# Kernel optimization log

Hardware: AMD Instinct MI355X
Metric: run time of the kernel (lower is better)

Reference implementation:

```python
import jax, jax.numpy as jnp
import numpy as np

# ---- static module configuration ----
N_POU = 16
N_BC = 3
P = N_POU + N_BC          # full_n_pou = 19
F = 3                      # n_fields
B, N, D_IN, D_Z, D_H = 16, 1024, 32, 64, 64
N_DIR = 64
MAX_ITERS = 50
ALPHA = 0.1                # damped fixed-point step of the nonlinear solver

# edge_pairs / delta_0 for the complete graph on P POU nodes (construct_delta0)
_ei, _ej = np.triu_indices(P, 1)
E = _ei.shape[0]           # n_one_forms = P*(P-1)/2 = 171
_d0 = np.zeros((E, P), np.float32)
_d0[np.arange(E), _ei] = -1.0
_d0[np.arange(E), _ej] = 1.0
DELTA0 = jnp.asarray(_d0)  # [E, P]
EI = jnp.asarray(_ei)
EJ = jnp.asarray(_ej)


def setup_inputs() -> dict:
    key = jax.random.key(0)
    ks = jax.random.split(key, 16)
    f32 = jnp.float32
    inp = {
        'in_tokens': jax.random.normal(ks[0], (B, N, D_IN), f32),
        'K_list': 0.02 * jax.random.normal(ks[1], (B, F, N, N), f32),
        'M_list': 0.02 * jax.random.normal(ks[2], (B, F, N, N), f32),
        'dirichlet_nodes': jax.random.randint(ks[3], (B, N_DIR), 0, N),
        'boundary_vals': jax.random.normal(ks[4], (B, N_DIR, F), f32),
        'u_init': jax.random.normal(ks[5], (B, P * F), f32),
        # learned parameters (encoder / source_model / boundary_w / flux_model)
        'W_enc': jax.random.normal(ks[6], (D_IN, D_Z), f32) / np.sqrt(D_IN),
        'b_enc': jnp.zeros((D_Z,), f32),
        'W_src': jax.random.normal(ks[7], (D_Z, F), f32) / np.sqrt(D_Z),
        'b_src': jnp.zeros((F,), f32),
        'W_pou': jax.random.normal(ks[8], (D_Z, P * F), f32) / np.sqrt(D_Z),
        'Wf1': jax.random.normal(ks[9], (2 * F, D_H), f32) / np.sqrt(2 * F),
        'Wz': jax.random.normal(ks[10], (D_Z, D_H), f32) / np.sqrt(D_Z),
        'bf': jnp.zeros((D_H,), f32),
        'Wf2': 0.1 * jax.random.normal(ks[11], (D_H, F), f32) / np.sqrt(D_H),
    }
    return inp


def reference(in_tokens, K_list, M_list, dirichlet_nodes, boundary_vals, u_init,
              W_enc, b_enc, W_src, b_src, W_pou, Wf1, Wz, bf, Wf2):
    Bc, Nn = in_tokens.shape[0], in_tokens.shape[1]
    latent_scaling = Nn / P

    # encoder: in_tokens -> per-node latents z [B,N,Dz]
    z = jnp.tanh(in_tokens @ W_enc + b_enc)

    # boundary_w: partition-of-unity weights W [B,P,N,F], boundary POUs biased
    # toward Dirichlet nodes via boundary_vals
    logits = (z @ W_pou).reshape(Bc, Nn, P, F)
    bidx = jnp.arange(Bc)[:, None]
    bvals_full = jnp.zeros((Bc, Nn, F), in_tokens.dtype).at[bidx, dirichlet_nodes].set(boundary_vals)
    logits = logits.at[:, :, P - N_BC:, :].add(bvals_full[:, :, None, :])
    Wmat = jax.nn.softmax(logits, axis=2).transpose(0, 2, 1, 3)  # [B,P,N,F]

    # source_model + latent projection (source_mode='identity' -> pass-through)
    f_full = z @ W_src + b_src                                    # [B,N,F]
    f_latent = jnp.einsum('bpif,bif->bpf', Wmat, f_full) / latent_scaling

    # project_bilinear_per_field: K_hat[b,p,q,f] = W K W^T / scaling
    def project(Kl):
        t = jnp.einsum('bpif,bfij->bpjf', Wmat, Kl)               # [B,P,N,F]
        return jnp.einsum('bpjf,bqjf->bpqf', t, Wmat) / latent_scaling

    # apply_dirichlet_per_field: boundary rows -> identity
    eyeP = jnp.eye(P, dtype=in_tokens.dtype)
    row_mask = jnp.zeros((P,), bool).at[P - N_BC:].set(True)
    def dirichlet_bilinear(Kh):
        return jnp.where(row_mask[None, :, None, None], eyeP[None, :, :, None], Kh)

    K_hat = dirichlet_bilinear(project(K_list))                   # [B,P,P,F]
    M_hat = dirichlet_bilinear(project(M_list))

    bc_mask = jnp.zeros((P, F), bool).at[P - N_BC:, :].set(True)
    bc_vals = jnp.zeros((P, F), in_tokens.dtype).at[P - N_BC, :].set(1.0)

    # flux_model conditioning: pooled latent, precomputed once
    zp = jnp.mean(z, axis=1) @ Wz                                 # [B,Dh]
    src_term = jnp.einsum('bpqf,bqf->bpf', M_hat, f_latent)       # constant in u

    def G(u_flat):  # G_residual
        u = u_flat.reshape(Bc, P, F)
        diff_term = jnp.einsum('bpqf,bqf->bpf', K_hat, u)
        ue = jnp.concatenate([u[:, EI], u[:, EJ]], axis=-1)       # [B,E,2F]
        flux = jnp.tanh(ue @ Wf1 + zp[:, None, :] + bf) @ Wf2     # [B,E,F]
        flux_term = jnp.einsum('ep,bef->bpf', DELTA0, flux)
        r = diff_term - src_term - flux_term
        r = jnp.where(bc_mask[None], u - bc_vals[None], r)        # Dirichlet residual
        return r.reshape(Bc, -1)

    # NonlinearSolver: damped fixed-point iteration, fixed MAX_ITERS under jit
    def step(u, _):
        return u - ALPHA * G(u), None
    u_hat, _ = jax.lax.scan(step, u_init, None, length=MAX_ITERS)

    u_coarse = u_hat.reshape(Bc, P, F)
    u_fine = jnp.einsum('bpif,bpf->bif', Wmat, u_coarse)          # [B,N,F]
    return u_fine
```

## Files before the change

kernel.cpp:

```cpp
#include <hip/hip_runtime.h>

#define Bn 16
#define Nn 1024
#define DIN 32
#define DZ 64
#define Fc 3
#define Pp 19
#define PPAD 20
#define Ee 171
#define ITERS 50
#define INV_SCALE (19.0f/1024.0f)
#define CHUNK 64
#define PF 4
#define PFK 8

#define OFF_WPROJ 0
#define OFF_FFULL 983040
#define OFF_FLAT  1033216
#define OFF_UBUF  1034128
#define OFF_BVALS 1035040
#define OFF_ZACC  1084192
#define OFF_KHAT  1085216
#define OFF_SRC   1099808
#define ZERO_FLOATS 65536
#define OFF_TPART 1100576
#define NEED_FLOATS (OFF_TPART + 48*16*16*1024)

__global__ __launch_bounds__(1024) void k_scatter(const int* __restrict__ nodes,
                                                  const float* __restrict__ bvals,
                                                  float* __restrict__ bfull) {
  __shared__ int sn[1024];
  int tid = threadIdx.x;
  sn[tid] = nodes[tid];
  __syncthreads();
  int b = tid >> 6, j = tid & 63;
  int node = sn[tid];
  bool win = true;
  for (int j2 = j + 1; j2 < 64; j2++)
    if (sn[(b << 6) | j2] == node) { win = false; break; }
  if (win) {
    #pragma unroll
    for (int f = 0; f < Fc; f++)
      bfull[((size_t)b*Nn + node)*Fc + f] = bvals[(size_t)tid*Fc + f];
  }
}

__global__ __launch_bounds__(128) void k_encode(
    const float* __restrict__ x, const float* __restrict__ Wenc, const float* __restrict__ benc,
    const float* __restrict__ Wsrc, const float* __restrict__ bsrc, const float* __restrict__ Wpou,
    const float* __restrict__ bfull, float* __restrict__ wproj, float* __restrict__ ffull,
    float* __restrict__ zacc) {
  __shared__ float sWenc[DIN*DZ];
  __shared__ float sWpou[DZ*57];
  __shared__ float sWsrc[DZ*Fc];
  int tid = threadIdx.x;
  for (int t = tid; t < DIN*DZ; t += 128) sWenc[t] = Wenc[t];
  for (int t = tid; t < DZ*57; t += 128) sWpou[t] = Wpou[t];
  for (int t = tid; t < DZ*Fc; t += 128) sWsrc[t] = Wsrc[t];
  __syncthreads();
  int g = blockIdx.x*128 + tid;
  int b = g >> 10, i = g & 1023;
  float xr[DIN];
  const float* xp = x + (size_t)g*DIN;
  #pragma unroll
  for (int k = 0; k < DIN; k += 4) {
    float4 t4 = *(const float4*)(xp + k);
    xr[k] = t4.x; xr[k+1] = t4.y; xr[k+2] = t4.z; xr[k+3] = t4.w;
  }
  float l[57];
  #pragma unroll
  for (int o = 0; o < 57; o++) l[o] = 0.f;
  float ff[3] = {bsrc[0], bsrc[1], bsrc[2]};
  int lane = tid & 63;
  for (int d = 0; d < DZ; d++) {
    float zd = benc[d];
    #pragma unroll
    for (int k = 0; k < DIN; k++) zd = fmaf(xr[k], sWenc[k*DZ + d], zd);
    zd = tanhf(zd);
    #pragma unroll
    for (int o = 0; o < 57; o++) l[o] = fmaf(zd, sWpou[d*57 + o], l[o]);
    #pragma unroll
    for (int f = 0; f < Fc; f++) ff[f] = fmaf(zd, sWsrc[d*Fc + f], ff[f]);
    float zs = zd;
    #pragma unroll
    for (int off = 32; off > 0; off >>= 1) zs += __shfl_xor(zs, off, 64);
    if (lane == 0) atomicAdd(&zacc[b*DZ + d], zs);
  }
  #pragma unroll
  for (int f = 0; f < Fc; f++) ffull[(size_t)g*Fc + f] = ff[f];
  #pragma unroll
  for (int f = 0; f < Fc; f++) {
    float bv = bfull[(size_t)g*Fc + f];
    l[16*3+f] += bv; l[17*3+f] += bv; l[18*3+f] += bv;
  }
  #pragma unroll
  for (int f = 0; f < Fc; f++) {
    float m = l[f];
    #pragma unroll
    for (int p = 1; p < Pp; p++) m = fmaxf(m, l[p*3+f]);
    float ex[Pp]; float s = 0.f;
    #pragma unroll
    for (int p = 0; p < Pp; p++) { ex[p] = __expf(l[p*3+f] - m); s += ex[p]; }
    float inv = 1.f / s;
    float* wp = wproj + ((size_t)(b*Fc + f)*Nn + i)*PPAD;
    #pragma unroll
    for (int p = 0; p < Pp; p++) wp[p] = ex[p]*inv;
  }
}

__global__ __launch_bounds__(256) void k_flat(const float* __restrict__ wproj,
                                              const float* __restrict__ ffull,
                                              float* __restrict__ flat) {
  int bf = blockIdx.x;
  int b = bf / 3, f = bf % 3;
  float acc[Pp];
  #pragma unroll
  for (int q = 0; q < Pp; q++) acc[q] = 0.f;
  for (int i = threadIdx.x; i < Nn; i += 256) {
    float fv = ffull[((size_t)b*Nn + i)*Fc + f];
    const float* row = wproj + ((size_t)bf*Nn + i)*PPAD;
    #pragma unroll
    for (int q = 0; q < Pp; q++) acc[q] = fmaf(row[q], fv, acc[q]);
  }
  #pragma unroll
  for (int q = 0; q < Pp; q++) {
    float v = acc[q];
    #pragma unroll
    for (int off = 32; off > 0; off >>= 1) v += __shfl_xor(v, off, 64);
    acc[q] = v;
  }
  __shared__ float red[4][Pp];
  int wave = threadIdx.x >> 6, lane = threadIdx.x & 63;
  if (lane == 0) {
    #pragma unroll
    for (int q = 0; q < Pp; q++) red[wave][q] = acc[q];
  }
  __syncthreads();
  if (threadIdx.x < Pp) {
    float s = red[0][threadIdx.x] + red[1][threadIdx.x] + red[2][threadIdx.x] + red[3][threadIdx.x];
    flat[bf*Pp + threadIdx.x] = s * INV_SCALE;
  }
}

__global__ __launch_bounds__(256, 3) void k_projT(
    const float* __restrict__ Kl, const float* __restrict__ wproj,
    float* __restrict__ tpart) {
  __shared__ float sW[16*CHUNK];
  int chunk = blockIdx.x;
  int bf = blockIdx.y;
  int i0 = chunk * CHUNK;
  const float* Kb = Kl + (size_t)bf*Nn*Nn + (size_t)i0*Nn;
  const float* Wrow0 = wproj + ((size_t)bf*Nn + i0)*PPAD;
  int tid = threadIdx.x;
  for (int t = tid; t < 16*CHUNK; t += 256) {
    int r = t & (CHUNK-1), p = t >> 6;
    sW[p*CHUNK + r] = Wrow0[r*PPAD + p];
  }
  __syncthreads();
  int j0 = tid * 4;
  float4 acc[16];
  #pragma unroll
  for (int p = 0; p < 16; p++) { acc[p].x = 0.f; acc[p].y = 0.f; acc[p].z = 0.f; acc[p].w = 0.f; }
  const float* kp = Kb + j0;
  float4 kbuf[PFK];
  #pragma unroll
  for (int s = 0; s < PFK; s++) kbuf[s] = *(const float4*)(kp + (size_t)s*Nn);
  for (int ii = 0; ii < CHUNK; ii += PFK) {
    #pragma unroll
    for (int s = 0; s < PFK; s++) {
      float4 k4 = kbuf[s];
      int nxt = (ii + PFK + s) & (CHUNK - 1);
      kbuf[s] = *(const float4*)(kp + (size_t)nxt*Nn);
      const float* wrow = &sW[ii + s];
      #pragma unroll
      for (int p = 0; p < 16; p++) {
        float wv = wrow[p*CHUNK];
        acc[p].x = fmaf(wv, k4.x, acc[p].x);
        acc[p].y = fmaf(wv, k4.y, acc[p].y);
        acc[p].z = fmaf(wv, k4.z, acc[p].z);
        acc[p].w = fmaf(wv, k4.w, acc[p].w);
      }
    }
  }
  float* tp = tpart + ((size_t)(bf*16 + chunk)*16)*Nn + j0;
  #pragma unroll
  for (int p = 0; p < 16; p++) *(float4*)(tp + (size_t)p*Nn) = acc[p];
}

__global__ __launch_bounds__(256, 3) void k_projM(
    const float* __restrict__ Ml, const float* __restrict__ wproj,
    const float* __restrict__ flat, float* __restrict__ srca) {
  __shared__ float sW[16*CHUNK];
  int chunk = blockIdx.x;
  int bf = blockIdx.y;
  int i0 = chunk * CHUNK;
  const float* Mb = Ml + (size_t)bf*Nn*Nn + (size_t)i0*Nn;
  const float* Wp = wproj + (size_t)bf*Nn*PPAD;
  const float* Wrow0 = Wp + (size_t)i0*PPAD;
  int tid = threadIdx.x;
  for (int t = tid; t < 16*CHUNK; t += 256) {
    int r = t & (CHUNK-1), p = t >> 6;
    sW[p*CHUNK + r] = Wrow0[r*PPAD + p];
  }
  float fl[Pp];
  #pragma unroll
  for (int q = 0; q < Pp; q++) fl[q] = flat[bf*Pp + q];
  int j0 = tid * 4;
  float v0, v1, v2, v3;
  {
    float vv[4];
    #pragma unroll
    for (int r = 0; r < 4; r++) {
      const float* row = Wp + (size_t)(j0 + r)*PPAD;
      float s = 0.f;
      #pragma unroll
      for (int q = 0; q < Pp; q++) s = fmaf(row[q], fl[q], s);
      vv[r] = s;
    }
    v0 = vv[0]; v1 = vv[1]; v2 = vv[2]; v3 = vv[3];
  }
  __syncthreads();
  float sa[16];
  #pragma unroll
  for (int p = 0; p < 16; p++) sa[p] = 0.f;
  const float* mp = Mb + j0;
  float4 mbuf[PFK];
  #pragma unroll
  for (int s = 0; s < PFK; s++) mbuf[s] = *(const float4*)(mp + (size_t)s*Nn);
  for (int ii = 0; ii < CHUNK; ii += PFK) {
    #pragma unroll
    for (int s = 0; s < PFK; s++) {
      float4 m4 = mbuf[s];
      int nxt = (ii + PFK + s) & (CHUNK - 1);
      mbuf[s] = *(const float4*)(mp + (size_t)nxt*Nn);
      float tm = m4.x*v0 + m4.y*v1 + m4.z*v2 + m4.w*v3;
      const float* wrow = &sW[ii + s];
      #pragma unroll
      for (int p = 0; p < 16; p++) sa[p] = fmaf(wrow[p*CHUNK], tm, sa[p]);
    }
  }
  int lane = tid & 63;
  #pragma unroll
  for (int p = 0; p < 16; p++) {
    float vq = sa[p];
    #pragma unroll
    for (int off = 32; off > 0; off >>= 1) vq += __shfl_xor(vq, off, 64);
    sa[p] = vq;
  }
  if (lane == 0) {
    #pragma unroll
    for (int p = 0; p < 16; p++) atomicAdd(&srca[bf*16 + p], sa[p] * INV_SCALE);
  }
}

__global__ __launch_bounds__(256) void k_khat(const float* __restrict__ tpart,
                                              const float* __restrict__ wproj,
                                              float* __restrict__ khat) {
  __shared__ float sT[16*64];
  __shared__ float sWq[64*PPAD];
  int jb = blockIdx.x, bf = blockIdx.y;
  int tid = threadIdx.x;
  {
    int id = tid * 4;
    int p = id >> 6;
    int r = id & 63;
    const float* base = tpart + ((size_t)(bf*16)*16 + p)*Nn + jb*64 + r;
    float4 s4 = make_float4(0.f, 0.f, 0.f, 0.f);
    #pragma unroll 4
    for (int c = 0; c < 16; c++) {
      float4 t4 = *(const float4*)(base + (size_t)c*16*Nn);
      s4.x += t4.x; s4.y += t4.y; s4.z += t4.z; s4.w += t4.w;
    }
    *(float4*)&sT[p*64 + r] = s4;
  }
  const float* wsrc = wproj + ((size_t)bf*Nn + jb*64)*PPAD;
  for (int t = tid; t < 64*PPAD; t += 256) sWq[t] = wsrc[t];
  __syncthreads();
  for (int o = tid; o < 16*Pp; o += 256) {
    int p = o / Pp, q = o - p*Pp;
    float s = 0.f;
    #pragma unroll
    for (int r = 0; r < 64; r++) s = fmaf(sT[p*64 + r], sWq[r*PPAD + q], s);
    atomicAdd(&khat[(bf*16 + p)*Pp + q], s * INV_SCALE);
  }
}

__global__ __launch_bounds__(256, 1) void k_project_fb(
    const float* __restrict__ Kl, const float* __restrict__ Ml,
    const float* __restrict__ wproj, const float* __restrict__ flat,
    float* __restrict__ khat, float* __restrict__ srca) {
  __shared__ float sW[16*CHUNK];
  int chunk = blockIdx.x;
  int bf = blockIdx.y;
  int i0 = chunk * CHUNK;
  const float* Kb = Kl + (size_t)bf*Nn*Nn + (size_t)i0*Nn;
  const float* Mb = Ml + (size_t)bf*Nn*Nn + (size_t)i0*Nn;
  const float* Wp = wproj + (size_t)bf*Nn*PPAD;
  const float* Wrow0 = Wp + (size_t)i0*PPAD;
  int tid = threadIdx.x;
  for (int t = tid; t < 16*CHUNK; t += 256) {
    int r = t & (CHUNK-1), p = t >> 6;
    sW[p*CHUNK + r] = Wrow0[r*PPAD + p];
  }
  float fl[Pp];
  #pragma unroll
  for (int q = 0; q < Pp; q++) fl[q] = flat[bf*Pp + q];
  int j0 = tid * 4;
  float v[4];
  #pragma unroll
  for (int r = 0; r < 4; r++) {
    const float* row = Wp + (size_t)(j0 + r)*PPAD;
    float s = 0.f;
    #pragma unroll
    for (int q = 0; q < Pp; q++) s = fmaf(row[q], fl[q], s);
    v[r] = s;
  }
  __syncthreads();
  float4 acc[16];
  float sa[16];
  #pragma unroll
  for (int p = 0; p < 16; p++) {
    acc[p].x = 0.f; acc[p].y = 0.f; acc[p].z = 0.f; acc[p].w = 0.f;
    sa[p] = 0.f;
  }
  const float* kp = Kb + j0;
  const float* mp = Mb + j0;
  float4 kbuf[PF], mbuf[PF];
  #pragma unroll
  for (int s = 0; s < PF; s++) {
    kbuf[s] = *(const float4*)(kp + (size_t)s*Nn);
    mbuf[s] = *(const float4*)(mp + (size_t)s*Nn);
  }
  for (int ii = 0; ii < CHUNK; ii += PF) {
    #pragma unroll
    for (int s = 0; s < PF; s++) {
      float4 k4 = kbuf[s], m4 = mbuf[s];
      int nxt = (ii + PF + s) & (CHUNK - 1);
      kbuf[s] = *(const float4*)(kp + (size_t)nxt*Nn);
      mbuf[s] = *(const float4*)(mp + (size_t)nxt*Nn);
      float tm = m4.x*v[0] + m4.y*v[1] + m4.z*v[2] + m4.w*v[3];
      const float* wrow = &sW[ii + s];
      #pragma unroll
      for (int p = 0; p < 16; p++) {
        float wv = wrow[p*CHUNK];
        acc[p].x = fmaf(wv, k4.x, acc[p].x);
        acc[p].y = fmaf(wv, k4.y, acc[p].y);
        acc[p].z = fmaf(wv, k4.z, acc[p].z);
        acc[p].w = fmaf(wv, k4.w, acc[p].w);
        sa[p] = fmaf(wv, tm, sa[p]);
      }
    }
  }
  int lane = tid & 63;
  #pragma unroll
  for (int q = 0; q < Pp; q++) {
    float w0 = Wp[(size_t)(j0 + 0)*PPAD + q];
    float w1 = Wp[(size_t)(j0 + 1)*PPAD + q];
    float w2 = Wp[(size_t)(j0 + 2)*PPAD + q];
    float w3 = Wp[(size_t)(j0 + 3)*PPAD + q];
    float pr[16];
    #pragma unroll
    for (int p = 0; p < 16; p++)
      pr[p] = acc[p].x*w0 + acc[p].y*w1 + acc[p].z*w2 + acc[p].w*w3;
    #pragma unroll
    for (int p = 0; p < 16; p++) {
      float vq = pr[p];
      #pragma unroll
      for (int off = 32; off > 0; off >>= 1) vq += __shfl_xor(vq, off, 64);
      pr[p] = vq;
    }
    if (lane == 0) {
      #pragma unroll
      for (int p = 0; p < 16; p++)
        atomicAdd(&khat[(bf*16 + p)*Pp + q], pr[p] * INV_SCALE);
    }
  }
  #pragma unroll
  for (int p = 0; p < 16; p++) {
    float vq = sa[p];
    #pragma unroll
    for (int off = 32; off > 0; off >>= 1) vq += __shfl_xor(vq, off, 64);
    sa[p] = vq;
  }
  if (lane == 0) {
    #pragma unroll
    for (int p = 0; p < 16; p++) atomicAdd(&srca[bf*16 + p], sa[p] * INV_SCALE);
  }
}

__global__ __launch_bounds__(384, 1) void k_solve(
    const float* __restrict__ khat, const float* __restrict__ srca,
    const float* __restrict__ zacc, const float* __restrict__ Wz,
    const float* __restrict__ u_init, const float* __restrict__ Wf1,
    const float* __restrict__ bfv, const float* __restrict__ Wf2,
    float* __restrict__ ubuf) {
  int b = blockIdx.x;
  __shared__ float u4[Pp*4];
  __shared__ float flux_s[Ee*Fc];
  __shared__ float sW1p[DZ*8];
  __shared__ float sW2p[DZ*4];
  __shared__ float sK[Fc*16*Pp];
  __shared__ float ssrc[Fc*16];
  int tid = threadIdx.x;
  for (int t = tid; t < 6*DZ; t += 384) {
    int k = t >> 6, d = t & 63;
    sW1p[d*8 + k] = 2.f * Wf1[t];
  }
  for (int t = tid; t < DZ*Fc; t += 384) {
    int d = t / 3, c = t - d*3;
    sW2p[d*4 + c] = Wf2[t];
  }
  if (tid < DZ) {
    float s = 0.f;
    for (int k = 0; k < DZ; k++) s = fmaf(zacc[b*DZ + k], Wz[k*DZ + tid], s);
    sW1p[tid*8 + 6] = 2.f * (bfv[tid] + s * (1.f/1024.f));
    sW1p[tid*8 + 7] = 0.f;
    sW2p[tid*4 + 3] = 0.f;
  }
  for (int t = tid; t < Fc*16*Pp; t += 384) sK[t] = khat[b*Fc*16*Pp + t];
  if (tid < 48) ssrc[tid] = srca[b*48 + tid];
  if (tid < 57) u4[(tid/3)*4 + (tid%3)] = u_init[b*57 + tid];
  if (tid < Pp) u4[tid*4 + 3] = 0.f;
  __syncthreads();
  int e = tid >> 1, h = tid & 1;
  bool active = (e < Ee);
  int ei = 0, ej = 0;
  if (active) {
    int r = e, i = 0;
    while (r >= 18 - i) { r -= 18 - i; i++; }
    ei = i; ej = i + 1 + r;
  }
  int d0 = h * 32;
  bool upd = (tid < 57);
  int up = tid / 3, uf = tid - (tid/3)*3;
  for (int it = 0; it < ITERS; it++) {
    if (active) {
      float4 ua = *(const float4*)&u4[ei*4];
      float4 ub = *(const float4*)&u4[ej*4];
      float fl0 = 0.f, fl1 = 0.f, fl2 = 0.f;
      #pragma unroll 16
      for (int dd = 0; dd < 32; dd++) {
        int d = d0 + dd;
        float4 wA = *(const float4*)&sW1p[d*8];
        float4 wB = *(const float4*)&sW1p[d*8 + 4];
        float pre = wB.z;
        pre = fmaf(ua.x, wA.x, pre);
        pre = fmaf(ua.y, wA.y, pre);
        pre = fmaf(ua.z, wA.z, pre);
        pre = fmaf(ub.x, wA.w, pre);
        pre = fmaf(ub.y, wB.x, pre);
        pre = fmaf(ub.z, wB.y, pre);
        float t = __expf(pre);
        float r = __builtin_amdgcn_rcpf(t + 1.f);
        float th = fmaf(-2.f, r, 1.f);
        float4 w2 = *(const float4*)&sW2p[d*4];
        fl0 = fmaf(th, w2.x, fl0);
        fl1 = fmaf(th, w2.y, fl1);
        fl2 = fmaf(th, w2.z, fl2);
      }
      fl0 += __shfl_xor(fl0, 1, 64);
      fl1 += __shfl_xor(fl1, 1, 64);
      fl2 += __shfl_xor(fl2, 1, 64);
      if (h == 0) { flux_s[e*3+0] = fl0; flux_s[e*3+1] = fl1; flux_s[e*3+2] = fl2; }
    }
    __syncthreads();
    if (upd) {
      float u_old = u4[up*4 + uf];
      float r_;
      if (up < 16) {
        float diff = 0.f;
        const float* kr = &sK[(uf*16 + up)*Pp];
        for (int q = 0; q < Pp; q++) diff = fmaf(kr[q], u4[q*4 + uf], diff);
        float ft = 0.f;
        for (int o = 0; o < Pp; o++) {
          if (o == up) continue;
          int i_ = (o < up) ? o : up;
          int j_ = (o < up) ? up : o;
          int eidx = i_*Pp - (i_*(i_+1))/2 + (j_ - i_ - 1);
          float sgn = (o < up) ? 1.f : -1.f;
          ft += sgn * flux_s[eidx*3 + uf];
        }
        r_ = diff - ssrc[uf*16 + up] - ft;
      } else {
        r_ = u_old - ((up == 16) ? 1.f : 0.f);
      }
      u4[up*4 + uf] = u_old - 0.1f * r_;
    }
    __syncthreads();
  }
  if (tid < 57) ubuf[b*57 + tid] = u4[(tid/3)*4 + (tid%3)];
}

__global__ __launch_bounds__(256) void k_out(const float* __restrict__ wproj,
                                             const float* __restrict__ ubuf,
                                             float* __restrict__ out) {
  __shared__ float u_s[57];
  int b = blockIdx.y;
  int i = blockIdx.x*256 + threadIdx.x;
  if (threadIdx.x < 57) u_s[threadIdx.x] = ubuf[b*57 + threadIdx.x];
  __syncthreads();
  #pragma unroll
  for (int f = 0; f < Fc; f++) {
    const float* row = wproj + ((size_t)(b*Fc + f)*Nn + i)*PPAD;
    float s = 0.f;
    #pragma unroll
    for (int p = 0; p < Pp; p++) s = fmaf(row[p], u_s[p*3 + f], s);
    out[((size_t)b*Nn + i)*Fc + f] = s;
  }
}

extern "C" void kernel_launch(void* const* d_in, const int* in_sizes, int n_in,
                              void* d_out, int out_size, void* d_ws, size_t ws_size,
                              hipStream_t stream) {
  const float* in_tokens = (const float*)d_in[0];
  const float* K_list    = (const float*)d_in[1];
  const float* M_list    = (const float*)d_in[2];
  const int*   dnodes    = (const int*)d_in[3];
  const float* bvals     = (const float*)d_in[4];
  const float* u_init    = (const float*)d_in[5];
  const float* W_enc     = (const float*)d_in[6];
  const float* b_enc     = (const float*)d_in[7];
  const float* W_src     = (const float*)d_in[8];
  const float* b_src     = (const float*)d_in[9];
  const float* W_pou     = (const float*)d_in[10];
  const float* Wf1       = (const float*)d_in[11];
  const float* Wz        = (const float*)d_in[12];
  const float* bfv       = (const float*)d_in[13];
  const float* Wf2       = (const float*)d_in[14];
  float* ws  = (float*)d_ws;
  float* out = (float*)d_out;

  float* WPROJ = ws + OFF_WPROJ;
  float* FFULL = ws + OFF_FFULL;
  float* FLAT  = ws + OFF_FLAT;
  float* UBUF  = ws + OFF_UBUF;
  float* BVALS = ws + OFF_BVALS;
  float* ZACC  = ws + OFF_ZACC;
  float* KHAT  = ws + OFF_KHAT;
  float* SRC   = ws + OFF_SRC;
  float* TPART = ws + OFF_TPART;

  hipMemsetAsync(ws + OFF_BVALS, 0, (size_t)ZERO_FLOATS * sizeof(float), stream);
  k_scatter<<<1, 1024, 0, stream>>>(dnodes, bvals, BVALS);
  k_encode<<<128, 128, 0, stream>>>(in_tokens, W_enc, b_enc, W_src, b_src, W_pou,
                                    BVALS, WPROJ, FFULL, ZACC);
  k_flat<<<Bn*Fc, 256, 0, stream>>>(WPROJ, FFULL, FLAT);
  if (ws_size >= (size_t)NEED_FLOATS * sizeof(float)) {
    k_projT<<<dim3(Nn/CHUNK, Bn*Fc), 256, 0, stream>>>(K_list, WPROJ, TPART);
    k_projM<<<dim3(Nn/CHUNK, Bn*Fc), 256, 0, stream>>>(M_list, WPROJ, FLAT, SRC);
    k_khat<<<dim3(16, Bn*Fc), 256, 0, stream>>>(TPART, WPROJ, KHAT);
  } else {
    k_project_fb<<<dim3(Nn/CHUNK, Bn*Fc), 256, 0, stream>>>(K_list, M_list, WPROJ, FLAT, KHAT, SRC);
  }
  k_solve<<<Bn, 384, 0, stream>>>(KHAT, SRC, ZACC, Wz, u_init, Wf1, bfv, Wf2, UBUF);
  k_out<<<dim3(Nn/256, Bn), 256, 0, stream>>>(WPROJ, UBUF, out);
}
```

Before: 787.7 us.

## Keep flux MLP weights in registers and split edges across 8-lane groups

The solve kernel now gives each lane a fixed 8-wide slice of the hidden dimension and keeps the Wf1, bias and Wf2 weights for that slice in registers. Each group of 8 lanes processes one edge per round, over 6 rounds, with a 3-step shuffle reduction. This removes the per-iteration LDS weight loads and shrinks the block from 384 to 256 threads. The residual loops are also unrolled. In exchange the kernel uses more registers and does more shuffles per edge, and some lanes sit idle in the last round.

```diff
diff --git a/kernel.cpp b/kernel.cpp
--- a/kernel.cpp
+++ b/kernel.cpp
@@ -388,7 +388,7 @@
   }
 }
 
-__global__ __launch_bounds__(384, 1) void k_solve(
+__global__ __launch_bounds__(256, 1) void k_solve(
     const float* __restrict__ khat, const float* __restrict__ srca,
     const float* __restrict__ zacc, const float* __restrict__ Wz,
     const float* __restrict__ u_init, const float* __restrict__ Wf1,
@@ -397,71 +397,84 @@
   int b = blockIdx.x;
   __shared__ float u4[Pp*4];
   __shared__ float flux_s[Ee*Fc];
-  __shared__ float sW1p[DZ*8];
-  __shared__ float sW2p[DZ*4];
+  __shared__ float sbz[DZ];
   __shared__ float sK[Fc*16*Pp];
   __shared__ float ssrc[Fc*16];
   int tid = threadIdx.x;
-  for (int t = tid; t < 6*DZ; t += 384) {
-    int k = t >> 6, d = t & 63;
-    sW1p[d*8 + k] = 2.f * Wf1[t];
-  }
-  for (int t = tid; t < DZ*Fc; t += 384) {
-    int d = t / 3, c = t - d*3;
-    sW2p[d*4 + c] = Wf2[t];
-  }
   if (tid < DZ) {
     float s = 0.f;
     for (int k = 0; k < DZ; k++) s = fmaf(zacc[b*DZ + k], Wz[k*DZ + tid], s);
-    sW1p[tid*8 + 6] = 2.f * (bfv[tid] + s * (1.f/1024.f));
-    sW1p[tid*8 + 7] = 0.f;
-    sW2p[tid*4 + 3] = 0.f;
-  }
-  for (int t = tid; t < Fc*16*Pp; t += 384) sK[t] = khat[b*Fc*16*Pp + t];
+    sbz[tid] = bfv[tid] + s * (1.f/1024.f);
+  }
+  for (int t = tid; t < Fc*16*Pp; t += 256) sK[t] = khat[b*Fc*16*Pp + t];
   if (tid < 48) ssrc[tid] = srca[b*48 + tid];
   if (tid < 57) u4[(tid/3)*4 + (tid%3)] = u_init[b*57 + tid];
   if (tid < Pp) u4[tid*4 + 3] = 0.f;
   __syncthreads();
-  int e = tid >> 1, h = tid & 1;
-  bool active = (e < Ee);
-  int ei = 0, ej = 0;
-  if (active) {
-    int r = e, i = 0;
+
+  int wave = tid >> 6, lane = tid & 63;
+  int g = lane >> 3, sub = lane & 7;
+  int dbase = sub * 8;
+  float w1r[6][8];
+  #pragma unroll
+  for (int k = 0; k < 6; k++)
+    #pragma unroll
+    for (int j = 0; j < 8; j++) w1r[k][j] = 2.f * Wf1[k*DZ + dbase + j];
+  float bzr[8];
+  #pragma unroll
+  for (int j = 0; j < 8; j++) bzr[j] = 2.f * sbz[dbase + j];
+  float w2r[3][8];
+  #pragma unroll
+  for (int j = 0; j < 8; j++) {
+    w2r[0][j] = Wf2[(dbase + j)*3 + 0];
+    w2r[1][j] = Wf2[(dbase + j)*3 + 1];
+    w2r[2][j] = Wf2[(dbase + j)*3 + 2];
+  }
+  int e_[6], ei_[6], ej_[6];
+  bool act_[6];
+  #pragma unroll
+  for (int rd = 0; rd < 6; rd++) {
+    int e = rd*32 + wave*8 + g;
+    act_[rd] = (e < Ee);
+    int r = act_[rd] ? e : 0, i = 0;
     while (r >= 18 - i) { r -= 18 - i; i++; }
-    ei = i; ej = i + 1 + r;
-  }
-  int d0 = h * 32;
+    e_[rd] = e; ei_[rd] = i; ej_[rd] = i + 1 + r;
+  }
   bool upd = (tid < 57);
   int up = tid / 3, uf = tid - (tid/3)*3;
+
   for (int it = 0; it < ITERS; it++) {
-    if (active) {
-      float4 ua = *(const float4*)&u4[ei*4];
-      float4 ub = *(const float4*)&u4[ej*4];
-      float fl0 = 0.f, fl1 = 0.f, fl2 = 0.f;
-      #pragma unroll 16
-      for (int dd = 0; dd < 32; dd++) {
-        int d = d0 + dd;
-        float4 wA = *(const float4*)&sW1p[d*8];
-        float4 wB = *(const float4*)&sW1p[d*8 + 4];
-        float pre = wB.z;
-        pre = fmaf(ua.x, wA.x, pre);
-        pre = fmaf(ua.y, wA.y, pre);
-        pre = fmaf(ua.z, wA.z, pre);
-        pre = fmaf(ub.x, wA.w, pre);
-        pre = fmaf(ub.y, wB.x, pre);
-        pre = fmaf(ub.z, wB.y, pre);
-        float t = __expf(pre);
-        float r = __builtin_amdgcn_rcpf(t + 1.f);
-        float th = fmaf(-2.f, r, 1.f);
-        float4 w2 = *(const float4*)&sW2p[d*4];
-        fl0 = fmaf(th, w2.x, fl0);
-        fl1 = fmaf(th, w2.y, fl1);
-        fl2 = fmaf(th, w2.z, fl2);
+    #pragma unroll
+    for (int rd = 0; rd < 6; rd++) {
+      if (act_[rd]) {
+        float4 ua = *(const float4*)&u4[ei_[rd]*4];
+        float4 ub = *(const float4*)&u4[ej_[rd]*4];
+        float fl0 = 0.f, fl1 = 0.f, fl2 = 0.f;
+        #pragma unroll
+        for (int j = 0; j < 8; j++) {
+          float pre = bzr[j];
+          pre = fmaf(ua.x, w1r[0][j], pre);
+          pre = fmaf(ua.y, w1r[1][j], pre);
+          pre = fmaf(ua.z, w1r[2][j], pre);
+          pre = fmaf(ub.x, w1r[3][j], pre);
+          pre = fmaf(ub.y, w1r[4][j], pre);
+          pre = fmaf(ub.z, w1r[5][j], pre);
+          float t = __expf(pre);
+          float rr = __builtin_amdgcn_rcpf(t + 1.f);
+          float th = fmaf(-2.f, rr, 1.f);
+          fl0 = fmaf(th, w2r[0][j], fl0);
+          fl1 = fmaf(th, w2r[1][j], fl1);
+          fl2 = fmaf(th, w2r[2][j], fl2);
+        }
+        fl0 += __shfl_xor(fl0, 1, 64); fl0 += __shfl_xor(fl0, 2, 64); fl0 += __shfl_xor(fl0, 4, 64);
+        fl1 += __shfl_xor(fl1, 1, 64); fl1 += __shfl_xor(fl1, 2, 64); fl1 += __shfl_xor(fl1, 4, 64);
+        fl2 += __shfl_xor(fl2, 1, 64); fl2 += __shfl_xor(fl2, 2, 64); fl2 += __shfl_xor(fl2, 4, 64);
+        if (sub == 0) {
+          flux_s[e_[rd]*3 + 0] = fl0;
+          flux_s[e_[rd]*3 + 1] = fl1;
+          flux_s[e_[rd]*3 + 2] = fl2;
+        }
       }
-      fl0 += __shfl_xor(fl0, 1, 64);
-      fl1 += __shfl_xor(fl1, 1, 64);
-      fl2 += __shfl_xor(fl2, 1, 64);
-      if (h == 0) { flux_s[e*3+0] = fl0; flux_s[e*3+1] = fl1; flux_s[e*3+2] = fl2; }
     }
     __syncthreads();
     if (upd) {
@@ -470,8 +483,10 @@
       if (up < 16) {
         float diff = 0.f;
         const float* kr = &sK[(uf*16 + up)*Pp];
+        #pragma unroll
         for (int q = 0; q < Pp; q++) diff = fmaf(kr[q], u4[q*4 + uf], diff);
         float ft = 0.f;
+        #pragma unroll
         for (int o = 0; o < Pp; o++) {
           if (o == up) continue;
           int i_ = (o < up) ? o : up;
@@ -552,6 +567,6 @@
   } else {
     k_project_fb<<<dim3(Nn/CHUNK, Bn*Fc), 256, 0, stream>>>(K_list, M_list, WPROJ, FLAT, KHAT, SRC);
   }
-  k_solve<<<Bn, 384, 0, stream>>>(KHAT, SRC, ZACC, Wz, u_init, Wf1, bfv, Wf2, UBUF);
+  k_solve<<<Bn, 256, 0, stream>>>(KHAT, SRC, ZACC, Wz, u_init, Wf1, bfv, Wf2, UBUF);
   k_out<<<dim3(Nn/256, Bn), 256, 0, stream>>>(WPROJ, UBUF, out);
 }
```

Measured after the change: 733.9 us. -6.8%, faster.

## Pack flux MLP weights per batch and read them as wave-uniform scalar loads

Applied to the files above, without the earlier changes.

A new small kernel precomputes the per-batch flux weights (Wf1, the conditioned bias and Wf2) into a packed 16-float-per-hidden-unit layout in global memory. The solver remaps threads so that each wave handles 64 edges over one half of the hidden dimension, making the weight address wave-uniform so it can be served by scalar loads instead of LDS reads. It also drops the cross-lane shuffle reduction, writing two partial flux buffers that the update step sums. The update loops are unrolled. This adds one kernel launch and depends on the compiler actually emitting scalar loads for the weights.

```diff
diff --git a/kernel.cpp b/kernel.cpp
--- a/kernel.cpp
+++ b/kernel.cpp
@@ -13,6 +13,7 @@
 #define CHUNK 64
 #define PF 4
 #define PFK 8
+#define WPACK_B 1024
 
 #define OFF_WPROJ 0
 #define OFF_FFULL 983040
@@ -23,7 +24,8 @@
 #define OFF_KHAT  1085216
 #define OFF_SRC   1099808
 #define ZERO_FLOATS 65536
-#define OFF_TPART 1100576
+#define OFF_WPACK 1100576
+#define OFF_TPART 1116960
 #define NEED_FLOATS (OFF_TPART + 48*16*16*1024)
 
 __global__ __launch_bounds__(1024) void k_scatter(const int* __restrict__ nodes,
@@ -140,6 +142,25 @@
     float s = red[0][threadIdx.x] + red[1][threadIdx.x] + red[2][threadIdx.x] + red[3][threadIdx.x];
     flat[bf*Pp + threadIdx.x] = s * INV_SCALE;
   }
+}
+
+__global__ __launch_bounds__(64) void k_wpack(
+    const float* __restrict__ zacc, const float* __restrict__ Wz,
+    const float* __restrict__ bfv, const float* __restrict__ Wf1,
+    const float* __restrict__ Wf2, float* __restrict__ wpack) {
+  int b = blockIdx.x, d = threadIdx.x;
+  float s = 0.f;
+  for (int k = 0; k < DZ; k++) s = fmaf(zacc[b*DZ + k], Wz[k*DZ + d], s);
+  float bz = bfv[d] + s * (1.f/1024.f);
+  float* w = wpack + (size_t)b*WPACK_B + d*16;
+  #pragma unroll
+  for (int k = 0; k < 6; k++) w[k] = 2.f * Wf1[k*DZ + d];
+  w[6] = 2.f * bz;
+  w[7] = 0.f;
+  w[8]  = Wf2[d*3 + 0];
+  w[9]  = Wf2[d*3 + 1];
+  w[10] = Wf2[d*3 + 2];
+  w[11] = 0.f; w[12] = 0.f; w[13] = 0.f; w[14] = 0.f; w[15] = 0.f;
 }
 
 __global__ __launch_bounds__(256, 3) void k_projT(
@@ -390,78 +411,63 @@
 
 __global__ __launch_bounds__(384, 1) void k_solve(
     const float* __restrict__ khat, const float* __restrict__ srca,
-    const float* __restrict__ zacc, const float* __restrict__ Wz,
-    const float* __restrict__ u_init, const float* __restrict__ Wf1,
-    const float* __restrict__ bfv, const float* __restrict__ Wf2,
+    const float* __restrict__ wpack, const float* __restrict__ u_init,
     float* __restrict__ ubuf) {
   int b = blockIdx.x;
   __shared__ float u4[Pp*4];
-  __shared__ float flux_s[Ee*Fc];
-  __shared__ float sW1p[DZ*8];
-  __shared__ float sW2p[DZ*4];
+  __shared__ float fluxp[2][Ee*3];
   __shared__ float sK[Fc*16*Pp];
   __shared__ float ssrc[Fc*16];
   int tid = threadIdx.x;
-  for (int t = tid; t < 6*DZ; t += 384) {
-    int k = t >> 6, d = t & 63;
-    sW1p[d*8 + k] = 2.f * Wf1[t];
-  }
-  for (int t = tid; t < DZ*Fc; t += 384) {
-    int d = t / 3, c = t - d*3;
-    sW2p[d*4 + c] = Wf2[t];
-  }
-  if (tid < DZ) {
-    float s = 0.f;
-    for (int k = 0; k < DZ; k++) s = fmaf(zacc[b*DZ + k], Wz[k*DZ + tid], s);
-    sW1p[tid*8 + 6] = 2.f * (bfv[tid] + s * (1.f/1024.f));
-    sW1p[tid*8 + 7] = 0.f;
-    sW2p[tid*4 + 3] = 0.f;
-  }
   for (int t = tid; t < Fc*16*Pp; t += 384) sK[t] = khat[b*Fc*16*Pp + t];
   if (tid < 48) ssrc[tid] = srca[b*48 + tid];
   if (tid < 57) u4[(tid/3)*4 + (tid%3)] = u_init[b*57 + tid];
   if (tid < Pp) u4[tid*4 + 3] = 0.f;
   __syncthreads();
-  int e = tid >> 1, h = tid & 1;
+
+  int wave = tid >> 6, lane = tid & 63;
+  int eg = wave % 3, dh = wave / 3;
+  int e = eg*64 + lane;
   bool active = (e < Ee);
   int ei = 0, ej = 0;
-  if (active) {
-    int r = e, i = 0;
+  {
+    int r = active ? e : 0, i = 0;
     while (r >= 18 - i) { r -= 18 - i; i++; }
     ei = i; ej = i + 1 + r;
   }
-  int d0 = h * 32;
+  const float* wpk = wpack + (size_t)b*WPACK_B
+                   + (size_t)__builtin_amdgcn_readfirstlane(dh * 32 * 16);
   bool upd = (tid < 57);
   int up = tid / 3, uf = tid - (tid/3)*3;
+
   for (int it = 0; it < ITERS; it++) {
     if (active) {
       float4 ua = *(const float4*)&u4[ei*4];
       float4 ub = *(const float4*)&u4[ej*4];
       float fl0 = 0.f, fl1 = 0.f, fl2 = 0.f;
-      #pragma unroll 16
+      #pragma unroll 8
       for (int dd = 0; dd < 32; dd++) {
-        int d = d0 + dd;
-        float4 wA = *(const float4*)&sW1p[d*8];
-        float4 wB = *(const float4*)&sW1p[d*8 + 4];
-        float pre = wB.z;
-        pre = fmaf(ua.x, wA.x, pre);
-        pre = fmaf(ua.y, wA.y, pre);
-        pre = fmaf(ua.z, wA.z, pre);
-        pre = fmaf(ub.x, wA.w, pre);
-        pre = fmaf(ub.y, wB.x, pre);
-        pre = fmaf(ub.z, wB.y, pre);
+        const float* s = wpk + dd*16;
+        float4 sA = *(const float4*)(s);
+        float4 sB = *(const float4*)(s + 4);
+        float4 sC = *(const float4*)(s + 8);
+        float pre = sB.z;
+        pre = fmaf(ua.x, sA.x, pre);
+        pre = fmaf(ua.y, sA.y, pre);
+        pre = fmaf(ua.z, sA.z, pre);
+        pre = fmaf(ub.x, sA.w, pre);
+        pre = fmaf(ub.y, sB.x, pre);
+        pre = fmaf(ub.z, sB.y, pre);
         float t = __expf(pre);
-        float r = __builtin_amdgcn_rcpf(t + 1.f);
-        float th = fmaf(-2.f, r, 1.f);
-        float4 w2 = *(const float4*)&sW2p[d*4];
-        fl0 = fmaf(th, w2.x, fl0);
-        fl1 = fmaf(th, w2.y, fl1);
-        fl2 = fmaf(th, w2.z, fl2);
+        float rr = __builtin_amdgcn_rcpf(t + 1.f);
+        float th = fmaf(-2.f, rr, 1.f);
+        fl0 = fmaf(th, sC.x, fl0);
+        fl1 = fmaf(th, sC.y, fl1);
+        fl2 = fmaf(th, sC.z, fl2);
       }
-      fl0 += __shfl_xor(fl0, 1, 64);
-      fl1 += __shfl_xor(fl1, 1, 64);
-      fl2 += __shfl_xor(fl2, 1, 64);
-      if (h == 0) { flux_s[e*3+0] = fl0; flux_s[e*3+1] = fl1; flux_s[e*3+2] = fl2; }
+      fluxp[dh][e*3 + 0] = fl0;
+      fluxp[dh][e*3 + 1] = fl1;
+      fluxp[dh][e*3 + 2] = fl2;
     }
     __syncthreads();
     if (upd) {
@@ -470,15 +476,17 @@
       if (up < 16) {
         float diff = 0.f;
         const float* kr = &sK[(uf*16 + up)*Pp];
+        #pragma unroll
         for (int q = 0; q < Pp; q++) diff = fmaf(kr[q], u4[q*4 + uf], diff);
         float ft = 0.f;
+        #pragma unroll
         for (int o = 0; o < Pp; o++) {
           if (o == up) continue;
           int i_ = (o < up) ? o : up;
           int j_ = (o < up) ? up : o;
           int eidx = i_*Pp - (i_*(i_+1))/2 + (j_ - i_ - 1);
           float sgn = (o < up) ? 1.f : -1.f;
-          ft += sgn * flux_s[eidx*3 + uf];
+          ft += sgn * (fluxp[0][eidx*3 + uf] + fluxp[1][eidx*3 + uf]);
         }
         r_ = diff - ssrc[uf*16 + up] - ft;
       } else {
@@ -538,12 +546,14 @@
   float* ZACC  = ws + OFF_ZACC;
   float* KHAT  = ws + OFF_KHAT;
   float* SRC   = ws + OFF_SRC;
+  float* WPACK = ws + OFF_WPACK;
   float* TPART = ws + OFF_TPART;
 
   hipMemsetAsync(ws + OFF_BVALS, 0, (size_t)ZERO_FLOATS * sizeof(float), stream);
   k_scatter<<<1, 1024, 0, stream>>>(dnodes, bvals, BVALS);
   k_encode<<<128, 128, 0, stream>>>(in_tokens, W_enc, b_enc, W_src, b_src, W_pou,
                                     BVALS, WPROJ, FFULL, ZACC);
+  k_wpack<<<Bn, 64, 0, stream>>>(ZACC, Wz, bfv, Wf1, Wf2, WPACK);
   k_flat<<<Bn*Fc, 256, 0, stream>>>(WPROJ, FFULL, FLAT);
   if (ws_size >= (size_t)NEED_FLOATS * sizeof(float)) {
     k_projT<<<dim3(Nn/CHUNK, Bn*Fc), 256, 0, stream>>>(K_list, WPROJ, TPART);
@@ -552,6 +562,6 @@
   } else {
     k_project_fb<<<dim3(Nn/CHUNK, Bn*Fc), 256, 0, stream>>>(K_list, M_list, WPROJ, FLAT, KHAT, SRC);
   }
-  k_solve<<<Bn, 384, 0, stream>>>(KHAT, SRC, ZACC, Wz, u_init, Wf1, bfv, Wf2, UBUF);
+  k_solve<<<Bn, 384, 0, stream>>>(KHAT, SRC, WPACK, u_init, UBUF);
   k_out<<<dim3(Nn/256, Bn), 256, 0, stream>>>(WPROJ, UBUF, out);
 }
```

New measurement: 733.6 us. 1.07x faster.
